# Kernel tuning notes

Measured on AMD Instinct MI355X. Metric: run time of the kernel, lower is better.

The kernel has to match this reference:

```python
import jax, jax.numpy as jnp
import numpy as np

TOP_K = 6
N_GROUP = 4
TOPK_GROUP = 2
ROUTED_SCALING = 2.5

T, H, E, I = 1024, 2048, 16, 704  # tokens, hidden, experts, expert ffn width
IS = 2 * I  # shared expert intermediate (n_shared_experts * moe_intermediate_size)


def setup_inputs() -> dict:
    key = jax.random.key(0)
    ks = jax.random.split(key, 6)
    s = 0.02
    return {
        "hidden_states": jax.random.normal(ks[0], (T, H), jnp.float32),
        "w_gate": jax.random.normal(ks[1], (H, E), jnp.float32) * s,
        "w_gate_up": jax.random.normal(ks[2], (E, H, 2 * I), jnp.float32) * s,
        "w_down": jax.random.normal(ks[3], (E, I, H), jnp.float32) * s,
        "w_shared_gate_up": jax.random.normal(ks[4], (H, 2 * IS), jnp.float32) * s,
        "w_shared_down": jax.random.normal(ks[5], (IS, H), jnp.float32) * s,
    }


def grouped_topk(scores, k, n_group, topk_group):
    # DeepSeek grouped top-k routing: pick topk_group expert groups by max
    # group score, mask out other groups, then top-k over remaining experts.
    t, e = scores.shape
    group_scores = scores.reshape(t, n_group, e // n_group).max(axis=-1)  # [T, G]
    _, gidx = jax.lax.top_k(group_scores, topk_group)                     # [T, kg]
    gmask = jax.nn.one_hot(gidx, n_group, dtype=scores.dtype).sum(axis=1)  # [T, G]
    smask = jnp.repeat(gmask, e // n_group, axis=1)                        # [T, E]
    masked = jnp.where(smask > 0, scores, 0.0)
    topk_w, topk_idx = jax.lax.top_k(masked, k)                            # [T, k]
    topk_w = topk_w / jnp.sum(topk_w, axis=-1, keepdims=True)              # renormalize
    return topk_w, topk_idx


def reference(hidden_states, w_gate, w_gate_up, w_down, w_shared_gate_up, w_shared_down):
    x = hidden_states                         # [T, H]
    t, e = x.shape[0], w_gate.shape[1]
    # router
    router_logits = x @ w_gate                # [T, E]
    scores = jax.nn.softmax(router_logits, axis=-1)
    topk_w, topk_idx = grouped_topk(scores, TOP_K, N_GROUP, TOPK_GROUP)
    combine = jnp.zeros((t, e), x.dtype).at[jnp.arange(t)[:, None], topk_idx].add(topk_w)
    # routed experts (dense-all-experts form, mathematically identical to dispatch)
    gu = jnp.einsum('th,ehi->tei', x, w_gate_up)        # [T, E, 2I]
    g, u = jnp.split(gu, 2, axis=-1)
    act = jax.nn.silu(g) * u                            # [T, E, I]
    act = act * combine[:, :, None]                     # apply routing weights
    routed = jnp.einsum('tei,eih->th', act, w_down) * ROUTED_SCALING
    # shared experts (SiLU gated MLP)
    sgu = x @ w_shared_gate_up
    sg, su = jnp.split(sgu, 2, axis=-1)
    shared = (jax.nn.silu(sg) * su) @ w_shared_down
    return routed + shared
```

## Files before the change

### kernel.cpp

```cpp
#include <hip/hip_runtime.h>

typedef unsigned short u16;
typedef u16 u16x8 __attribute__((ext_vector_type(8)));
typedef __bf16 bf16x8 __attribute__((ext_vector_type(8)));
typedef float f32x4 __attribute__((ext_vector_type(4)));

#define T_TOK 1024
#define H_DIM 2048
#define E_NUM 16
#define I_DIM 704
#define IS_DIM 1408

#define MFMA(a, b, c) __builtin_amdgcn_mfma_f32_16x16x32_bf16(a, b, c, 0, 0, 0)

__device__ __forceinline__ u16 f2bf(float f) {
  union { float f; unsigned u; } v; v.f = f;
  unsigned r = v.u + 0x7fffu + ((v.u >> 16) & 1u);
  return (u16)(r >> 16);
}

__device__ __forceinline__ void gload16(const void* g, void* l) {
  __builtin_amdgcn_global_load_lds(
      (const __attribute__((address_space(1))) unsigned int*)g,
      (__attribute__((address_space(3))) unsigned int*)l, 16, 0, 0);
}

__device__ __forceinline__ const char* lds_sw(const u16* base, int row, int kByte) {
  return (const char*)base + row * 128 + (kByte ^ ((row & 7) << 4));
}

__device__ __forceinline__ void transp64_body(const float* __restrict__ in,
                                              u16* __restrict__ outp, int R, int C,
                                              int cx, int ry, int z, char* SM) {
  float (*tile)[65] = (float(*)[65])SM;
  const size_t base = (size_t)z * (size_t)R * C;
  const int c0 = cx * 64, r0 = ry * 64;
  const int tid = threadIdx.x;
  const int c4 = (tid & 15) * 4, rb = tid >> 4;
#pragma unroll
  for (int i = 0; i < 4; ++i) {
    const int row = i * 16 + rb;
    const f32x4 v = *(const f32x4*)(in + base + (size_t)(r0 + row) * C + c0 + c4);
    tile[row][c4 + 0] = v[0];
    tile[row][c4 + 1] = v[1];
    tile[row][c4 + 2] = v[2];
    tile[row][c4 + 3] = v[3];
  }
  __syncthreads();
#pragma unroll
  for (int i = 0; i < 8; ++i) {
    const int idx = i * 256 + tid;
    const int oc = idx >> 5, pr = idx & 31;
    const unsigned lo = f2bf(tile[2 * pr][oc]);
    const unsigned hi = f2bf(tile[2 * pr + 1][oc]);
    *(unsigned*)&outp[base + (size_t)(c0 + oc) * R + r0 + 2 * pr] = lo | (hi << 16);
  }
}

__global__ __launch_bounds__(256) void router_k(const float* __restrict__ x,
                                                const float* __restrict__ wg,
                                                float* __restrict__ comb,
                                                u16* __restrict__ XB) {
  const int t = blockIdx.x;
  const int tid = threadIdx.x;
  const float* xr = x + (size_t)t * H_DIM;
  const int h0 = tid * 8;
  f32x4 a = *(const f32x4*)(xr + h0);
  f32x4 b = *(const f32x4*)(xr + h0 + 4);
  u16x8 o;
  o[0] = f2bf(a[0]); o[1] = f2bf(a[1]); o[2] = f2bf(a[2]); o[3] = f2bf(a[3]);
  o[4] = f2bf(b[0]); o[5] = f2bf(b[1]); o[6] = f2bf(b[2]); o[7] = f2bf(b[3]);
  *(u16x8*)(XB + (size_t)t * H_DIM + h0) = o;

  float acc[E_NUM];
#pragma unroll
  for (int e = 0; e < E_NUM; ++e) acc[e] = 0.f;
#pragma unroll
  for (int j = 0; j < 8; ++j) {
    const float xv = j < 4 ? a[j] : b[j - 4];
    const f32x4* wr = (const f32x4*)(wg + (size_t)(h0 + j) * E_NUM);
#pragma unroll
    for (int q = 0; q < 4; ++q) {
      f32x4 w4 = wr[q];
      acc[q * 4 + 0] += xv * w4[0];
      acc[q * 4 + 1] += xv * w4[1];
      acc[q * 4 + 2] += xv * w4[2];
      acc[q * 4 + 3] += xv * w4[3];
    }
  }
#pragma unroll
  for (int e = 0; e < E_NUM; ++e)
    for (int off = 32; off > 0; off >>= 1) acc[e] += __shfl_down(acc[e], off);
  __shared__ float part[4][E_NUM];
  if ((tid & 63) == 0) {
#pragma unroll
    for (int e = 0; e < E_NUM; ++e) part[tid >> 6][e] = acc[e];
  }
  __syncthreads();
  if (tid == 0) {
    float p[E_NUM];
    float mx = -1e30f;
    for (int e = 0; e < E_NUM; ++e) {
      p[e] = part[0][e] + part[1][e] + part[2][e] + part[3][e];
      mx = fmaxf(mx, p[e]);
    }
    float s = 0.f;
    for (int e = 0; e < E_NUM; ++e) { p[e] = __expf(p[e] - mx); s += p[e]; }
    const float invs = 1.f / s;
    for (int e = 0; e < E_NUM; ++e) p[e] *= invs;
    float gs[4];
    for (int g = 0; g < 4; ++g)
      gs[g] = fmaxf(fmaxf(p[4 * g], p[4 * g + 1]), fmaxf(p[4 * g + 2], p[4 * g + 3]));
    int g1 = 0;
    for (int g = 1; g < 4; ++g) if (gs[g] > gs[g1]) g1 = g;
    int g2 = -1;
    for (int g = 0; g < 4; ++g) {
      if (g == g1) continue;
      if (g2 < 0 || gs[g] > gs[g2]) g2 = g;
    }
    float m2[E_NUM], cw[E_NUM];
    for (int e = 0; e < E_NUM; ++e) {
      int g = e >> 2;
      m2[e] = (g == g1 || g == g2) ? p[e] : 0.f;
      cw[e] = 0.f;
    }
    float sum6 = 0.f;
    for (int k = 0; k < 6; ++k) {
      int bi = 0; float bv = -1.f;
      for (int e = 0; e < E_NUM; ++e)
        if (m2[e] > bv) { bv = m2[e]; bi = e; }
      cw[bi] = bv; sum6 += bv; m2[bi] = -2.f;
    }
    const float scale = 2.5f / sum6;
    for (int e = 0; e < E_NUM; ++e) comb[t * E_NUM + e] = cw[e] * scale;
  }
}

__global__ __launch_bounds__(256) void dispatch_k(const float* __restrict__ comb,
                                                  int* __restrict__ cnt,
                                                  int* __restrict__ tok) {
  const int e = blockIdx.x;
  const int tid = threadIdx.x;
  const int lane = tid & 63, wid = tid >> 6;
  __shared__ int wtot[4];
  int running = 0;
  for (int chunk = 0; chunk < T_TOK / 256; ++chunk) {
    const int t = chunk * 256 + tid;
    const bool sel = comb[t * E_NUM + e] > 0.f;
    unsigned long long mask = __ballot(sel);
    const int pre = __popcll(mask & ((1ull << lane) - 1ull));
    if (lane == 0) wtot[wid] = __popcll(mask);
    __syncthreads();
    int wbase = running;
    for (int w = 0; w < wid; ++w) wbase += wtot[w];
    if (sel) tok[e * T_TOK + wbase + pre] = t;
    running += wtot[0] + wtot[1] + wtot[2] + wtot[3];
    __syncthreads();
  }
  if (tid == 0) cnt[e] = running;
}

#define TGU_WGU_BLKS (22 * 32 * 16)
__global__ __launch_bounds__(256) void transp_gu_k(const float* __restrict__ wgu,
                                                   const float* __restrict__ wsgu,
                                                   u16* __restrict__ WGUT,
                                                   u16* __restrict__ WSGUT) {
  __shared__ __align__(16) char SM[16640];
  const int bid = blockIdx.x;
  if (bid < TGU_WGU_BLKS) {
    transp64_body(wgu, WGUT, H_DIM, 2 * I_DIM, bid % 22, (bid / 22) % 32, bid / 704, SM);
  } else {
    const int id = bid - TGU_WGU_BLKS;
    transp64_body(wsgu, WSGUT, H_DIM, 2 * IS_DIM, id % 44, id / 44, 0, SM);
  }
}

__device__ __forceinline__ void gu_body(
    const u16* __restrict__ A, const u16* __restrict__ Bt,
    const float* __restrict__ comb, const int* __restrict__ cnt,
    const int* __restrict__ tok, u16* __restrict__ outp,
    int gu_off, long long bt_e_stride, long long out_e_stride, int out_stride,
    int bx, int by, int e, char* SM) {
  const int M = cnt ? cnt[e] : T_TOK;
  const int m0 = by * 128;
  if (m0 >= M) return;
  u16* S = (u16*)SM;

  const int n0 = bx * 64;
  const u16* Bte = Bt + (size_t)e * bt_e_stride;
  const u16* Bgp = Bte + (size_t)n0 * H_DIM;
  const u16* Bup = Bte + (size_t)(gu_off + n0) * H_DIM;
  const int tid = threadIdx.x;
  const int w = tid >> 6, l = tid & 63;
  const int r8 = l >> 3;
  const int sk = ((l & 7) ^ r8) * 8;

  size_t arow[4];
#pragma unroll
  for (int j = 0; j < 4; ++j) {
    const int m = m0 + w * 32 + j * 8 + r8;
    const int mc = m < M ? m : M - 1;
    const int t = tok ? tok[e * T_TOK + mc] : mc;
    arow[j] = (size_t)t * H_DIM + sk;
  }

  const int wr = tid >> 7;
  const int wc = (tid >> 6) & 1;
  const int fr = l & 15;
  const int fg = l >> 4;

  const f32x4 zero = {0.f, 0.f, 0.f, 0.f};
  f32x4 accg[4][2], accu[4][2];
#pragma unroll
  for (int i = 0; i < 4; ++i)
#pragma unroll
    for (int j = 0; j < 2; ++j) { accg[i][j] = zero; accu[i][j] = zero; }

  for (int kt = 0; kt < H_DIM / 64; ++kt) {
    const int k0 = kt * 64;
#pragma unroll
    for (int j = 0; j < 4; ++j)
      gload16(A + arow[j] + k0, S + (w * 4 + j) * 512);
#pragma unroll
    for (int j = 0; j < 2; ++j) {
      const size_t br = (size_t)(w * 16 + j * 8 + r8) * H_DIM + sk + k0;
      gload16(Bgp + br, S + 8192 + (w * 2 + j) * 512);
      gload16(Bup + br, S + 12288 + (w * 2 + j) * 512);
    }
    __syncthreads();
    const u16* AsC = S;
    const u16* BgC = S + 8192;
    const u16* BuC = S + 12288;
#pragma unroll
    for (int kk = 0; kk < 2; ++kk) {
      const int kb = kk * 64 + fg * 16;
      bf16x8 af[4], bg[2], bu[2];
#pragma unroll
      for (int mi = 0; mi < 4; ++mi)
        af[mi] = *(const bf16x8*)lds_sw(AsC, wr * 64 + mi * 16 + fr, kb);
#pragma unroll
      for (int ni = 0; ni < 2; ++ni) {
        bg[ni] = *(const bf16x8*)lds_sw(BgC, wc * 32 + ni * 16 + fr, kb);
        bu[ni] = *(const bf16x8*)lds_sw(BuC, wc * 32 + ni * 16 + fr, kb);
      }
#pragma unroll
      for (int mi = 0; mi < 4; ++mi)
#pragma unroll
        for (int ni = 0; ni < 2; ++ni) {
          accg[mi][ni] = MFMA(af[mi], bg[ni], accg[mi][ni]);
          accu[mi][ni] = MFMA(af[mi], bu[ni], accu[mi][ni]);
        }
    }
    __syncthreads();
  }

  const int colb = n0 + wc * 32;
#pragma unroll
  for (int mi = 0; mi < 4; ++mi) {
#pragma unroll
    for (int r = 0; r < 4; ++r) {
      const int ml = wr * 64 + mi * 16 + fg * 4 + r;
      if (m0 + ml >= M) continue;
      const int trow = tok ? tok[e * T_TOK + m0 + ml] : (m0 + ml);
      const float wgt = comb ? comb[trow * E_NUM + e] : 1.0f;
      const size_t rowoff = (size_t)e * out_e_stride + (size_t)(m0 + ml) * out_stride;
#pragma unroll
      for (int ni = 0; ni < 2; ++ni) {
        float g = accg[mi][ni][r];
        float u = accu[mi][ni][r];
        float sg = g / (1.f + __expf(-g));
        outp[rowoff + colb + ni * 16 + fr] = f2bf(sg * u * wgt);
      }
    }
  }
}

#define MG_GUR_BLKS (11 * 8 * 16)
#define MG_GUS_BLKS (22 * 8)
#define MG_TWD_BLKS (32 * 11 * 16)
#define MG_TWSD_BLKS (32 * 22)
__global__ __launch_bounds__(256, 4) void mega_k(
    const u16* __restrict__ XB, const u16* __restrict__ WGUT,
    const u16* __restrict__ WSGUT, const float* __restrict__ comb,
    const int* __restrict__ cnt, const int* __restrict__ tok,
    u16* __restrict__ ACTC, u16* __restrict__ ACTS,
    const float* __restrict__ wd, const float* __restrict__ wsd,
    u16* __restrict__ WDT, u16* __restrict__ WSDT) {
  __shared__ __align__(16) char SM[32768];
  const int bid = blockIdx.x;
  if (bid < MG_GUR_BLKS) {
    gu_body(XB, WGUT, comb, cnt, tok, ACTC, I_DIM, (long long)(2 * I_DIM) * H_DIM,
            (long long)T_TOK * I_DIM, I_DIM, bid % 11, (bid / 11) % 8, bid / 88, SM);
  } else if (bid < MG_GUR_BLKS + MG_GUS_BLKS) {
    const int id = bid - MG_GUR_BLKS;
    gu_body(XB, WSGUT, nullptr, nullptr, nullptr, ACTS, IS_DIM, 0, 0, IS_DIM,
            id % 22, id / 22, 0, SM);
  } else if (bid < MG_GUR_BLKS + MG_GUS_BLKS + MG_TWD_BLKS) {
    const int id = bid - MG_GUR_BLKS - MG_GUS_BLKS;
    transp64_body(wd, WDT, I_DIM, H_DIM, id % 32, (id / 32) % 11, id / 352, SM);
  } else {
    const int id = bid - MG_GUR_BLKS - MG_GUS_BLKS - MG_TWD_BLKS;
    transp64_body(wsd, WSDT, IS_DIM, H_DIM, id % 32, id / 32, 0, SM);
  }
}

template <bool ATOMIC>
__device__ __forceinline__ void down_core(
    const u16* __restrict__ Ap, int astride,
    const u16* __restrict__ Bp, int bstride,
    int NT, int M, int m0, int n0, const int* tokS, float* __restrict__ outp) {
  __shared__ __align__(16) u16 S[12288];
  const int tid = threadIdx.x;
  const int w = tid >> 6, l = tid & 63;
  const int r8 = l >> 3;
  const int sk = ((l & 7) ^ r8) * 8;

  size_t arow[2];
#pragma unroll
  for (int j = 0; j < 2; ++j) {
    const int m = w * 16 + j * 8 + r8;
    arow[j] = (size_t)(m0 + m < M ? m : (M - 1 - m0 > 0 ? M - 1 - m0 : 0)) * astride + sk;
  }
  size_t brow[4];
#pragma unroll
  for (int j = 0; j < 4; ++j)
    brow[j] = (size_t)(w * 32 + j * 8 + r8) * bstride + sk;

  auto STAGE = [&](int kt) {
    const int k0 = kt * 64;
#pragma unroll
    for (int j = 0; j < 2; ++j)
      gload16(Ap + arow[j] + k0, S + (w * 2 + j) * 512);
#pragma unroll
    for (int j = 0; j < 4; ++j)
      gload16(Bp + brow[j] + k0, S + 4096 + (w * 4 + j) * 512);
  };

  const int fr = l & 15, fg = l >> 4;
  const f32x4 zero = {0.f, 0.f, 0.f, 0.f};
  f32x4 acc[4][2];
#pragma unroll
  for (int i = 0; i < 4; ++i)
#pragma unroll
    for (int j = 0; j < 2; ++j) acc[i][j] = zero;

  for (int kt = 0; kt < NT; ++kt) {
    STAGE(kt);
    __syncthreads();
    const u16* AsC = S;
    const u16* BsC = S + 4096;
#pragma unroll
    for (int kk = 0; kk < 2; ++kk) {
      const int kb = kk * 64 + fg * 16;
      bf16x8 af[4], bfr[2];
#pragma unroll
      for (int mi = 0; mi < 4; ++mi)
        af[mi] = *(const bf16x8*)lds_sw(AsC, mi * 16 + fr, kb);
#pragma unroll
      for (int ni = 0; ni < 2; ++ni)
        bfr[ni] = *(const bf16x8*)lds_sw(BsC, w * 32 + ni * 16 + fr, kb);
#pragma unroll
      for (int mi = 0; mi < 4; ++mi)
#pragma unroll
        for (int ni = 0; ni < 2; ++ni) acc[mi][ni] = MFMA(af[mi], bfr[ni], acc[mi][ni]);
    }
    __syncthreads();
  }

#pragma unroll
  for (int mi = 0; mi < 4; ++mi) {
#pragma unroll
    for (int r = 0; r < 4; ++r) {
      const int ml = mi * 16 + fg * 4 + r;
      if (m0 + ml >= M) continue;
      const int trow = ATOMIC ? tokS[ml] : (m0 + ml);
      float* op = outp + (size_t)trow * H_DIM + n0 + w * 32;
#pragma unroll
      for (int ni = 0; ni < 2; ++ni) {
        if (ATOMIC)
          atomicAdd(op + ni * 16 + fr, acc[mi][ni][r]);
        else
          op[ni * 16 + fr] = acc[mi][ni][r];
      }
    }
  }
}

__global__ __launch_bounds__(256, 4) void down_shared_k(
    const u16* __restrict__ A1, const u16* __restrict__ B1t, float* __restrict__ outp) {
  const int n0 = blockIdx.x * 128, m0 = blockIdx.y * 64;
  down_core<false>(A1 + (size_t)m0 * IS_DIM, IS_DIM, B1t + (size_t)n0 * IS_DIM, IS_DIM,
                   IS_DIM / 64, T_TOK, m0, n0, nullptr, outp);
}

__global__ __launch_bounds__(256, 4) void down_routed_k(
    const u16* __restrict__ ACTC, const u16* __restrict__ WDT,
    const int* __restrict__ cnt, const int* __restrict__ tok, float* __restrict__ outp) {
  const int e = blockIdx.z;
  const int M = cnt[e];
  const int m0 = blockIdx.y * 64;
  if (m0 >= M) return;
  const int n0 = blockIdx.x * 128;
  __shared__ int tokS[64];
  const int tid = threadIdx.x;
  if (tid < 64) tokS[tid] = tok[e * T_TOK + (m0 + tid < M ? m0 + tid : M - 1)];
  __syncthreads();
  down_core<true>(ACTC + ((size_t)e * T_TOK + m0) * I_DIM, I_DIM,
                  WDT + ((size_t)e * H_DIM + n0) * I_DIM, I_DIM,
                  I_DIM / 64, M, m0, n0, tokS, outp);
}

extern "C" void kernel_launch(void* const* d_in, const int* in_sizes, int n_in,
                              void* d_out, int out_size, void* d_ws, size_t ws_size,
                              hipStream_t stream) {
  const float* x    = (const float*)d_in[0];
  const float* wg   = (const float*)d_in[1];
  const float* wgu  = (const float*)d_in[2];
  const float* wd   = (const float*)d_in[3];
  const float* wsgu = (const float*)d_in[4];
  const float* wsd  = (const float*)d_in[5];
  float* out = (float*)d_out;

  char* ws = (char*)d_ws;
  size_t off = 0;
  auto alloc = [&](size_t b) { size_t r = off; off += (b + 255) & ~(size_t)255; return r; };
  u16*   XB    = (u16*)  (ws + alloc((size_t)T_TOK * H_DIM * 2));
  float* COMB  = (float*)(ws + alloc((size_t)T_TOK * E_NUM * 4));
  int*   CNT   = (int*)  (ws + alloc((size_t)E_NUM * 4));
  int*   TOK   = (int*)  (ws + alloc((size_t)E_NUM * T_TOK * 4));
  u16*   WGUT  = (u16*)  (ws + alloc((size_t)E_NUM * 2 * I_DIM * H_DIM * 2));
  u16*   WDT   = (u16*)  (ws + alloc((size_t)E_NUM * H_DIM * I_DIM * 2));
  u16*   WSGUT = (u16*)  (ws + alloc((size_t)2 * IS_DIM * H_DIM * 2));
  u16*   WSDT  = (u16*)  (ws + alloc((size_t)H_DIM * IS_DIM * 2));
  u16*   ACTC  = (u16*)  (ws + alloc((size_t)E_NUM * T_TOK * I_DIM * 2));
  u16*   ACTS  = (u16*)  (ws + alloc((size_t)T_TOK * IS_DIM * 2));
  if (ws_size < off) return;

  router_k<<<T_TOK, 256, 0, stream>>>(x, wg, COMB, XB);
  dispatch_k<<<E_NUM, 256, 0, stream>>>(COMB, CNT, TOK);
  transp_gu_k<<<TGU_WGU_BLKS + 32 * 44, 256, 0, stream>>>(wgu, wsgu, WGUT, WSGUT);
  mega_k<<<MG_GUR_BLKS + MG_GUS_BLKS + MG_TWD_BLKS + MG_TWSD_BLKS, 256, 0, stream>>>(
      XB, WGUT, WSGUT, COMB, CNT, TOK, ACTC, ACTS, wd, wsd, WDT, WSDT);
  down_shared_k<<<dim3(H_DIM / 128, T_TOK / 64), 256, 0, stream>>>(ACTS, WSDT, out);
  down_routed_k<<<dim3(H_DIM / 128, T_TOK / 64, E_NUM), 256, 0, stream>>>(
      ACTC, WDT, CNT, TOK, out);
}
```

Baseline: 260.0 us.

## Fuse router with weight transposes and merge shared/routed down-projection launches

Merges the router and the gate/up weight-transpose kernels into one launch that also zeroes the output buffer. The shared-expert and routed-expert down projections now run in a single launch that accumulates atomically, with the shared expert as an extra z-slice. The intent is to cut launch overhead and the serial gap between the two down-projection kernels so their blocks overlap. In exchange, shared-expert output now goes through atomic adds instead of plain stores, and the extra zeroing pass adds memory traffic.

Result: faster. 251.3 us (-3.3%).

```diff
diff --git a/kernel.cpp b/kernel.cpp
--- a/kernel.cpp
+++ b/kernel.cpp
@@ -57,11 +57,10 @@
   }
 }
 
-__global__ __launch_bounds__(256) void router_k(const float* __restrict__ x,
-                                                const float* __restrict__ wg,
-                                                float* __restrict__ comb,
-                                                u16* __restrict__ XB) {
-  const int t = blockIdx.x;
+__device__ __forceinline__ void router_body(const float* __restrict__ x,
+                                            const float* __restrict__ wg,
+                                            float* __restrict__ comb,
+                                            u16* __restrict__ XB, int t, char* SM) {
   const int tid = threadIdx.x;
   const float* xr = x + (size_t)t * H_DIM;
   const int h0 = tid * 8;
@@ -91,7 +90,7 @@
 #pragma unroll
   for (int e = 0; e < E_NUM; ++e)
     for (int off = 32; off > 0; off >>= 1) acc[e] += __shfl_down(acc[e], off);
-  __shared__ float part[4][E_NUM];
+  float (*part)[E_NUM] = (float(*)[E_NUM])SM;
   if ((tid & 63) == 0) {
 #pragma unroll
     for (int e = 0; e < E_NUM; ++e) part[tid >> 6][e] = acc[e];
@@ -136,6 +135,33 @@
   }
 }
 
+#define FP_ROUTER T_TOK
+#define FP_ZERO 512
+#define FP_WGU (22 * 32 * 16)
+#define FP_WSGU (44 * 32)
+__global__ __launch_bounds__(256) void fused_pre_k(
+    const float* __restrict__ x, const float* __restrict__ wg,
+    float* __restrict__ comb, u16* __restrict__ XB,
+    const float* __restrict__ wgu, const float* __restrict__ wsgu,
+    u16* __restrict__ WGUT, u16* __restrict__ WSGUT, float* __restrict__ outz) {
+  __shared__ __align__(16) char SM[16640];
+  const int bid = blockIdx.x;
+  if (bid < FP_ROUTER) {
+    router_body(x, wg, comb, XB, bid, SM);
+  } else if (bid < FP_ROUTER + FP_ZERO) {
+    const int i = ((bid - FP_ROUTER) * 256 + threadIdx.x) * 16;
+    const f32x4 z = {0.f, 0.f, 0.f, 0.f};
+#pragma unroll
+    for (int j = 0; j < 4; ++j) *(f32x4*)(outz + i + j * 4) = z;
+  } else if (bid < FP_ROUTER + FP_ZERO + FP_WGU) {
+    const int id = bid - FP_ROUTER - FP_ZERO;
+    transp64_body(wgu, WGUT, H_DIM, 2 * I_DIM, id % 22, (id / 22) % 32, id / 704, SM);
+  } else {
+    const int id = bid - FP_ROUTER - FP_ZERO - FP_WGU;
+    transp64_body(wsgu, WSGUT, H_DIM, 2 * IS_DIM, id % 44, id / 44, 0, SM);
+  }
+}
+
 __global__ __launch_bounds__(256) void dispatch_k(const float* __restrict__ comb,
                                                   int* __restrict__ cnt,
                                                   int* __restrict__ tok) {
@@ -158,21 +184,6 @@
     __syncthreads();
   }
   if (tid == 0) cnt[e] = running;
-}
-
-#define TGU_WGU_BLKS (22 * 32 * 16)
-__global__ __launch_bounds__(256) void transp_gu_k(const float* __restrict__ wgu,
-                                                   const float* __restrict__ wsgu,
-                                                   u16* __restrict__ WGUT,
-                                                   u16* __restrict__ WSGUT) {
-  __shared__ __align__(16) char SM[16640];
-  const int bid = blockIdx.x;
-  if (bid < TGU_WGU_BLKS) {
-    transp64_body(wgu, WGUT, H_DIM, 2 * I_DIM, bid % 22, (bid / 22) % 32, bid / 704, SM);
-  } else {
-    const int id = bid - TGU_WGU_BLKS;
-    transp64_body(wsgu, WSGUT, H_DIM, 2 * IS_DIM, id % 44, id / 44, 0, SM);
-  }
 }
 
 __device__ __forceinline__ void gu_body(
@@ -304,8 +315,7 @@
   }
 }
 
-template <bool ATOMIC>
-__device__ __forceinline__ void down_core(
+__device__ __forceinline__ void down_core_atomic(
     const u16* __restrict__ Ap, int astride,
     const u16* __restrict__ Bp, int bstride,
     int NT, int M, int m0, int n0, const int* tokS, float* __restrict__ outp) {
@@ -326,16 +336,6 @@
   for (int j = 0; j < 4; ++j)
     brow[j] = (size_t)(w * 32 + j * 8 + r8) * bstride + sk;
 
-  auto STAGE = [&](int kt) {
-    const int k0 = kt * 64;
-#pragma unroll
-    for (int j = 0; j < 2; ++j)
-      gload16(Ap + arow[j] + k0, S + (w * 2 + j) * 512);
-#pragma unroll
-    for (int j = 0; j < 4; ++j)
-      gload16(Bp + brow[j] + k0, S + 4096 + (w * 4 + j) * 512);
-  };
-
   const int fr = l & 15, fg = l >> 4;
   const f32x4 zero = {0.f, 0.f, 0.f, 0.f};
   f32x4 acc[4][2];
@@ -345,7 +345,13 @@
     for (int j = 0; j < 2; ++j) acc[i][j] = zero;
 
   for (int kt = 0; kt < NT; ++kt) {
-    STAGE(kt);
+    const int k0 = kt * 64;
+#pragma unroll
+    for (int j = 0; j < 2; ++j)
+      gload16(Ap + arow[j] + k0, S + (w * 2 + j) * 512);
+#pragma unroll
+    for (int j = 0; j < 4; ++j)
+      gload16(Bp + brow[j] + k0, S + 4096 + (w * 4 + j) * 512);
     __syncthreads();
     const u16* AsC = S;
     const u16* BsC = S + 4096;
@@ -373,41 +379,40 @@
     for (int r = 0; r < 4; ++r) {
       const int ml = mi * 16 + fg * 4 + r;
       if (m0 + ml >= M) continue;
-      const int trow = ATOMIC ? tokS[ml] : (m0 + ml);
-      float* op = outp + (size_t)trow * H_DIM + n0 + w * 32;
-#pragma unroll
-      for (int ni = 0; ni < 2; ++ni) {
-        if (ATOMIC)
-          atomicAdd(op + ni * 16 + fr, acc[mi][ni][r]);
-        else
-          op[ni * 16 + fr] = acc[mi][ni][r];
-      }
-    }
-  }
-}
-
-__global__ __launch_bounds__(256, 4) void down_shared_k(
-    const u16* __restrict__ A1, const u16* __restrict__ B1t, float* __restrict__ outp) {
-  const int n0 = blockIdx.x * 128, m0 = blockIdx.y * 64;
-  down_core<false>(A1 + (size_t)m0 * IS_DIM, IS_DIM, B1t + (size_t)n0 * IS_DIM, IS_DIM,
-                   IS_DIM / 64, T_TOK, m0, n0, nullptr, outp);
-}
-
-__global__ __launch_bounds__(256, 4) void down_routed_k(
+      float* op = outp + (size_t)tokS[ml] * H_DIM + n0 + w * 32;
+#pragma unroll
+      for (int ni = 0; ni < 2; ++ni)
+        atomicAdd(op + ni * 16 + fr, acc[mi][ni][r]);
+    }
+  }
+}
+
+__global__ __launch_bounds__(256, 4) void down_all_k(
     const u16* __restrict__ ACTC, const u16* __restrict__ WDT,
-    const int* __restrict__ cnt, const int* __restrict__ tok, float* __restrict__ outp) {
+    const u16* __restrict__ ACTS, const u16* __restrict__ WSDT,
+    const int* __restrict__ cnt, const int* __restrict__ tok,
+    float* __restrict__ outp) {
   const int e = blockIdx.z;
-  const int M = cnt[e];
+  const bool shared = (e == E_NUM);
+  const int M = shared ? T_TOK : cnt[e];
   const int m0 = blockIdx.y * 64;
   if (m0 >= M) return;
   const int n0 = blockIdx.x * 128;
   __shared__ int tokS[64];
   const int tid = threadIdx.x;
-  if (tid < 64) tokS[tid] = tok[e * T_TOK + (m0 + tid < M ? m0 + tid : M - 1)];
+  if (tid < 64) {
+    const int m = m0 + tid;
+    tokS[tid] = shared ? m : tok[e * T_TOK + (m < M ? m : M - 1)];
+  }
   __syncthreads();
-  down_core<true>(ACTC + ((size_t)e * T_TOK + m0) * I_DIM, I_DIM,
-                  WDT + ((size_t)e * H_DIM + n0) * I_DIM, I_DIM,
-                  I_DIM / 64, M, m0, n0, tokS, outp);
+  if (shared)
+    down_core_atomic(ACTS + (size_t)m0 * IS_DIM, IS_DIM,
+                     WSDT + (size_t)n0 * IS_DIM, IS_DIM,
+                     IS_DIM / 64, M, m0, n0, tokS, outp);
+  else
+    down_core_atomic(ACTC + ((size_t)e * T_TOK + m0) * I_DIM, I_DIM,
+                     WDT + ((size_t)e * H_DIM + n0) * I_DIM, I_DIM,
+                     I_DIM / 64, M, m0, n0, tokS, outp);
 }
 
 extern "C" void kernel_launch(void* const* d_in, const int* in_sizes, int n_in,
@@ -436,12 +441,11 @@
   u16*   ACTS  = (u16*)  (ws + alloc((size_t)T_TOK * IS_DIM * 2));
   if (ws_size < off) return;
 
-  router_k<<<T_TOK, 256, 0, stream>>>(x, wg, COMB, XB);
+  fused_pre_k<<<FP_ROUTER + FP_ZERO + FP_WGU + FP_WSGU, 256, 0, stream>>>(
+      x, wg, COMB, XB, wgu, wsgu, WGUT, WSGUT, out);
   dispatch_k<<<E_NUM, 256, 0, stream>>>(COMB, CNT, TOK);
-  transp_gu_k<<<TGU_WGU_BLKS + 32 * 44, 256, 0, stream>>>(wgu, wsgu, WGUT, WSGUT);
   mega_k<<<MG_GUR_BLKS + MG_GUS_BLKS + MG_TWD_BLKS + MG_TWSD_BLKS, 256, 0, stream>>>(
       XB, WGUT, WSGUT, COMB, CNT, TOK, ACTC, ACTS, wd, wsd, WDT, WSDT);
-  down_shared_k<<<dim3(H_DIM / 128, T_TOK / 64), 256, 0, stream>>>(ACTS, WSDT, out);
-  down_routed_k<<<dim3(H_DIM / 128, T_TOK / 64, E_NUM), 256, 0, stream>>>(
-      ACTC, WDT, CNT, TOK, out);
-}
+  down_all_k<<<dim3(H_DIM / 128, T_TOK / 64, E_NUM + 1), 256, 0, stream>>>(
+      ACTC, WDT, ACTS, WSDT, CNT, TOK, out);
+}
```
